# Performance work log

Hardware: AMD Instinct MI355X
Metric: run time of the kernel (lower is better)

## Reference

```python
import jax, jax.numpy as jnp
import numpy as np

# Graph geometry: G complete graphs (molecules) of n nodes each.
N_PER_G, G, DEG = 64, 256, 16
H, D = 8, 8
IN_DIM = H * D      # 64
EDGE_DIM = 64
N = N_PER_G * G                      # 16384 nodes
EF = G * N_PER_G * N_PER_G           # 1,048,576 full edges
ES = G * N_PER_G * DEG               # 262,144 sparse edges
SCALE = float(np.sqrt(D))


def _edges():
    n = N_PER_G
    # full graph: all (i -> j) pairs per block, edge id = b*n*n + i*n + j
    ij = np.arange(n * n)
    i, j = ij // n, ij % n
    b = np.arange(G)[:, None]
    src_full = (b * n + i[None, :]).reshape(-1).astype(np.int32)
    dst_full = (b * n + j[None, :]).reshape(-1).astype(np.int32)
    # sparse graph: each dst j receives from DEG distinct sources (j+1..j+DEG mod n)
    jj = np.arange(n)[:, None]
    kk = np.arange(DEG)[None, :]
    ii = (jj + 1 + kk) % n
    eid_block = (ii * n + jj).reshape(-1)                 # [n*DEG]
    sparse_eid = (np.arange(G)[:, None] * n * n + eid_block[None, :]).reshape(-1).astype(np.int32)
    return jnp.asarray(src_full), jnp.asarray(dst_full), jnp.asarray(sparse_eid)


def setup_inputs() -> dict:
    key = jax.random.key(0)
    ks = jax.random.split(key, 16)
    w = lambda k, shape, s=0.05: s * jax.random.normal(k, shape, jnp.float32)
    src_full, dst_full, sparse_eid = _edges()
    return dict(
        h=jax.random.normal(ks[0], (N, IN_DIM), jnp.float32),
        e=jax.random.normal(ks[1], (ES, EDGE_DIM), jnp.float32),
        adj2=jax.random.uniform(ks[2], (EF,), jnp.float32),
        rel_pos_3d=jax.random.normal(ks[3], (EF, H), jnp.float32),
        Wq=w(ks[4], (H * D, IN_DIM)), bq=jnp.zeros((H * D,), jnp.float32),
        Wk=w(ks[5], (H * D, IN_DIM)), bk=jnp.zeros((H * D,), jnp.float32),
        Wv=w(ks[6], (H * D, IN_DIM)), bv=jnp.zeros((H * D,), jnp.float32),
        Wpe=w(ks[7], (H, EDGE_DIM)), bpe=jnp.zeros((H,), jnp.float32),
        Wap=w(ks[8], (EDGE_DIM, H)), bap=jnp.zeros((EDGE_DIM,), jnp.float32),
        Wo=w(ks[9], (H * D, H * D)), bo=jnp.zeros((H * D,), jnp.float32),
        Woe=w(ks[10], (EDGE_DIM, EDGE_DIM)), boe=jnp.zeros((EDGE_DIM,), jnp.float32),
        src_full=src_full, dst_full=dst_full, sparse_eid=sparse_eid,
    )


def reference(h, e, adj2, rel_pos_3d, Wq, bq, Wk, bk, Wv, bv, Wpe, bpe,
              Wap, bap, Wo, bo, Woe, boe, src_full, dst_full, sparse_eid):
    Qh = (h @ Wq.T + bq).reshape(N, H, D)
    Kh = (h @ Wk.T + bk).reshape(N, H, D)
    Vh = (h @ Wv.T + bv).reshape(N, H, D)
    proj_e = e @ Wpe.T + bpe                                   # [ES, H]
    # edge-wise QK dot (src=K, dst=Q), scaled, then gaussian-decay + rel-pos bias
    score = jnp.sum(Kh[src_full] * Qh[dst_full], axis=-1) / SCALE   # [EF, H]
    score = score * adj2[:, None] + rel_pos_3d                      # [EF, H]
    # gather sparse-subgraph scores, project for edge output, add proj_e bias
    sc_sp = score[sparse_eid]                                        # [ES, H]
    e_out_raw = sc_sp @ Wap.T + bap                                  # [ES, EDGE_DIM]
    score = score.at[sparse_eid].set(sc_sp + proj_e)
    # edge softmax over incoming edges of each destination node
    logits = jnp.clip(score, -5.0, 5.0)
    m = jax.ops.segment_max(logits, dst_full, num_segments=N)
    ex = jnp.exp(logits - m[dst_full])
    den = jax.ops.segment_sum(ex, dst_full, num_segments=N)
    attn = ex / den[dst_full]                                        # [EF, H]
    # weighted scatter-sum of source values
    wV = jax.ops.segment_sum(Vh[src_full] * attn[..., None], dst_full, num_segments=N)
    h_out = wV.reshape(N, H * D) @ Wo.T + bo
    e_out = (e_out_raw + e) @ Woe.T + boe
    return h_out, e_out
```

## Files before the change

### kernel.cpp

```cpp
#include <hip/hip_runtime.h>


__global__ __launch_bounds__(512, 2) void qkvpe_kernel(
    const float* __restrict__ h,
    const float* __restrict__ e,
    const float* __restrict__ Wq, const float* __restrict__ bq,
    const float* __restrict__ Wk, const float* __restrict__ bk,
    const float* __restrict__ Wv, const float* __restrict__ bv,
    const float* __restrict__ Wpe, const float* __restrict__ bpe,
    float* __restrict__ Qs, float* __restrict__ Ks, float* __restrict__ Vs,
    float* __restrict__ PEs)
{
    const int t = threadIdx.x;
    if (blockIdx.x < 256) {
        const int b    = blockIdx.x;
        const int lane = t & 63;
        const int wu   = __builtin_amdgcn_readfirstlane(t >> 6);
        const float* hrow = h + (size_t)(b * 64 + lane) * 64;
        float accQ[8], accK[8], accV[8];
        #pragma unroll
        for (int cc = 0; cc < 8; ++cc) {
            const int c = wu * 8 + cc;
            accQ[cc] = bq[c]; accK[cc] = bk[c]; accV[cc] = bv[c];
        }
        #pragma unroll 1
        for (int k0 = 0; k0 < 4; ++k0) {
            float hv[16];
            #pragma unroll
            for (int u = 0; u < 4; ++u) {
                const float4 x = ((const float4*)hrow)[k0 * 4 + u];
                hv[u*4+0] = x.x; hv[u*4+1] = x.y; hv[u*4+2] = x.z; hv[u*4+3] = x.w;
            }
            #pragma unroll
            for (int cc = 0; cc < 8; ++cc) {
                const int c = wu * 8 + cc;
                const float* wq  = Wq + c * 64 + k0 * 16;
                const float* wk  = Wk + c * 64 + k0 * 16;
                const float* wvp = Wv + c * 64 + k0 * 16;
                #pragma unroll
                for (int k = 0; k < 16; ++k) {
                    accQ[cc] = fmaf(hv[k], wq[k],  accQ[cc]);
                    accK[cc] = fmaf(hv[k], wk[k],  accK[cc]);
                    accV[cc] = fmaf(hv[k], wvp[k], accV[cc]);
                }
            }
        }
        const size_t o = (size_t)(b * 64 + lane) * 64 + wu * 8;
        *(float4*)(Qs + o)     = make_float4(accQ[0], accQ[1], accQ[2], accQ[3]);
        *(float4*)(Qs + o + 4) = make_float4(accQ[4], accQ[5], accQ[6], accQ[7]);
        *(float4*)(Ks + o)     = make_float4(accK[0], accK[1], accK[2], accK[3]);
        *(float4*)(Ks + o + 4) = make_float4(accK[4], accK[5], accK[6], accK[7]);
        *(float4*)(Vs + o)     = make_float4(accV[0], accV[1], accV[2], accV[3]);
        *(float4*)(Vs + o + 4) = make_float4(accV[4], accV[5], accV[6], accV[7]);
    } else {
        const int row = (blockIdx.x - 256) * 512 + t;
        const float* erow = e + (size_t)row * 64;
        float acc[8];
        #pragma unroll
        for (int h2 = 0; h2 < 8; ++h2) acc[h2] = bpe[h2];
        #pragma unroll 1
        for (int k0 = 0; k0 < 4; ++k0) {
            float ev[16];
            #pragma unroll
            for (int u = 0; u < 4; ++u) {
                const float4 x = ((const float4*)erow)[k0 * 4 + u];
                ev[u*4+0] = x.x; ev[u*4+1] = x.y; ev[u*4+2] = x.z; ev[u*4+3] = x.w;
            }
            #pragma unroll
            for (int h2 = 0; h2 < 8; ++h2) {
                const float* wp = Wpe + h2 * 64 + k0 * 16;
                #pragma unroll
                for (int k = 0; k < 16; ++k)
                    acc[h2] = fmaf(ev[k], wp[k], acc[h2]);
            }
        }
        float* p0 = PEs + (size_t)row * 8;
        *(float4*)(p0)     = make_float4(acc[0], acc[1], acc[2], acc[3]);
        *(float4*)(p0 + 4) = make_float4(acc[4], acc[5], acc[6], acc[7]);
    }
}

__global__ __launch_bounds__(512, 2) void attn_kernel(
    const float* __restrict__ Qs, const float* __restrict__ Ks,
    const float* __restrict__ Vs, const float* __restrict__ PEs,
    const float* __restrict__ adj2,
    const float* __restrict__ rel,
    const float* __restrict__ Wo, const float* __restrict__ bo,
    float* __restrict__ h_out,
    float* __restrict__ scsp)
{
    __shared__ float shK[64 * 64];
    __shared__ float shV[64 * 64];
    __shared__ float shPE[512 * 8];

    const int b2   = blockIdx.x;
    const int b    = b2 >> 1;
    const int joff = (b2 & 1) << 5;
    const int t    = threadIdx.x;

    const int j_local = t >> 4;
    const int hh      = (t >> 1) & 7;
    const int half    = t & 1;
    const int j       = joff + j_local;

    const float* adjB = adj2 + (size_t)b * 4096 + j;
    const float* relB = rel  + ((size_t)b * 4096 + j) * 8 + hh;
    float A[32], R[32];
    #pragma unroll
    for (int it = 0; it < 32; ++it) {
        const int i = (half << 5) + it;
        A[it] = adjB[(size_t)i * 64];
        R[it] = relB[(size_t)i * 512];
    }

    {
        const int r = t >> 3, g = t & 7;
        const int d = r * 64 + ((g ^ (r & 7)) << 3);
        const float* kp = Ks + (size_t)b * 4096 + t * 8;
        const float* vp = Vs + (size_t)b * 4096 + t * 8;
        *(float4*)&shK[d]     = *(const float4*)(kp);
        *(float4*)&shK[d + 4] = *(const float4*)(kp + 4);
        *(float4*)&shV[d]     = *(const float4*)(vp);
        *(float4*)&shV[d + 4] = *(const float4*)(vp + 4);
        const float* pp = PEs + ((size_t)b * 1024 + joff * 16 + t) * 8;
        *(float4*)&shPE[t * 8]     = *(const float4*)(pp);
        *(float4*)&shPE[t * 8 + 4] = *(const float4*)(pp + 4);
    }
    float q[8];
    {
        const float* qp = Qs + (size_t)(b * 64 + j) * 64 + hh * 8;
        const float4 a = *(const float4*)qp;
        const float4 c = *(const float4*)(qp + 4);
        q[0]=a.x; q[1]=a.y; q[2]=a.z; q[3]=a.w;
        q[4]=c.x; q[5]=c.y; q[6]=c.z; q[7]=c.w;
    }
    __syncthreads();

    float den = 0.f;
    float wv[8] = {0.f,0.f,0.f,0.f,0.f,0.f,0.f,0.f};
    const float inv_scale = 0.35355339059327379f;
    #pragma unroll 4
    for (int it = 0; it < 32; ++it) {
        const int i  = (half << 5) + it;
        const int kb = i * 64 + ((hh ^ (i & 7)) << 3);
        const float4 kA = *(const float4*)&shK[kb];
        const float4 kB = *(const float4*)&shK[kb + 4];
        float s;
        s = kA.x * q[0];
        s = fmaf(kA.y, q[1], s); s = fmaf(kA.z, q[2], s); s = fmaf(kA.w, q[3], s);
        s = fmaf(kB.x, q[4], s); s = fmaf(kB.y, q[5], s); s = fmaf(kB.z, q[6], s);
        s = fmaf(kB.w, q[7], s);
        s = fmaf(s * inv_scale, A[it], R[it]);
        const int kidx = (i - j - 1) & 63;
        if (kidx < 16) {
            const int x = (j_local * 16 + kidx) * 8 + hh;
            const float pe = shPE[x];
            shPE[x] = s;
            s += pe;
        }
        s = fminf(fmaxf(s, -5.f), 5.f);
        const float ex = __expf(s);
        den += ex;
        const float4 vA = *(const float4*)&shV[kb];
        const float4 vB = *(const float4*)&shV[kb + 4];
        wv[0] = fmaf(ex, vA.x, wv[0]); wv[1] = fmaf(ex, vA.y, wv[1]);
        wv[2] = fmaf(ex, vA.z, wv[2]); wv[3] = fmaf(ex, vA.w, wv[3]);
        wv[4] = fmaf(ex, vB.x, wv[4]); wv[5] = fmaf(ex, vB.y, wv[5]);
        wv[6] = fmaf(ex, vB.z, wv[6]); wv[7] = fmaf(ex, vB.w, wv[7]);
    }
    den += __shfl_xor(den, 1);
    #pragma unroll
    for (int u = 0; u < 8; ++u) wv[u] += __shfl_xor(wv[u], 1);
    __syncthreads();

    {
        const float4 a = *(const float4*)&shPE[t * 8];
        const float4 c = *(const float4*)&shPE[t * 8 + 4];
        float* sp = scsp + (size_t)((size_t)b * 1024 + joff * 16 + t) * 8;
        *(float4*)(sp)     = a;
        *(float4*)(sp + 4) = c;
    }
    if (half == 0) {
        const float id = 1.f / den;
        float* wp = &shK[j_local * 64 + hh * 8];
        *(float4*)(wp)     = make_float4(wv[0]*id, wv[1]*id, wv[2]*id, wv[3]*id);
        *(float4*)(wp + 4) = make_float4(wv[4]*id, wv[5]*id, wv[6]*id, wv[7]*id);
    }
    __syncthreads();

    {
        const int rl = t >> 4;
        const int cq = t & 15;
        float acc[4];
        #pragma unroll
        for (int u = 0; u < 4; ++u) acc[u] = bo[cq * 4 + u];
        float tv[64];
        #pragma unroll
        for (int v = 0; v < 16; ++v) {
            const float4 x = *(const float4*)&shK[rl * 64 + v * 4];
            tv[v*4+0] = x.x; tv[v*4+1] = x.y; tv[v*4+2] = x.z; tv[v*4+3] = x.w;
        }
        #pragma unroll
        for (int u = 0; u < 4; ++u) {
            const float* wo = Wo + (cq * 4 + u) * 64;
            #pragma unroll
            for (int k = 0; k < 64; ++k)
                acc[u] = fmaf(tv[k], wo[k], acc[u]);
        }
        float* orow = h_out + (size_t)(b * 64 + joff + rl) * 64 + cq * 4;
        *(float4*)orow = make_float4(acc[0], acc[1], acc[2], acc[3]);
    }
}

__global__ void prep_kernel(const float* __restrict__ Wap, const float* __restrict__ bap,
                            const float* __restrict__ Woe, const float* __restrict__ boe,
                            float* __restrict__ M2)
{
    const int t = blockIdx.x * 64 + threadIdx.x;
    if (t < 512) {
        const int c = t >> 3, hq = t & 7;
        float s = 0.f;
        #pragma unroll 8
        for (int k = 0; k < 64; ++k) s = fmaf(Woe[c * 64 + k], Wap[k * 8 + hq], s);
        M2[t] = s;
    } else if (t < 576) {
        const int c = t - 512;
        float s = boe[c];
        #pragma unroll 8
        for (int k = 0; k < 64; ++k) s = fmaf(bap[k], Woe[t * 64 + k], s);
        M2[512 + c] = s;
    }
}

__global__ __launch_bounds__(256, 2) void eout_kernel(
    const float* __restrict__ e,
    const float* __restrict__ scsp,
    const float* __restrict__ Woe,
    const float* __restrict__ M2g,
    float* __restrict__ e_out)
{
    __shared__ float shE[64 * 64];
    __shared__ float shS[64 * 8];

    const int t    = threadIdx.x;
    const int base = blockIdx.x * 64;

    {
        const int r = t >> 2, qq = t & 3;
        const float* ep = e + (size_t)(base + r) * 64 + qq * 16;
        #pragma unroll
        for (int u = 0; u < 4; ++u) {
            const float4 x = ((const float4*)ep)[u];
            const int cc = qq * 4 + u;
            *(float4*)&shE[r * 64 + ((cc ^ (r & 15)) << 2)] = x;
        }
    }
    if (t < 128) {
        const int r = t >> 1, pp = t & 1;
        *(float4*)&shS[r * 8 + pp * 4] =
            *(const float4*)(scsp + (size_t)(base + r) * 8 + pp * 4);
    }
    __syncthreads();

    const int w = __builtin_amdgcn_readfirstlane(t >> 6);
    const int r = t & 63;

    float ev[64];
    #pragma unroll
    for (int v = 0; v < 16; ++v) {
        const float4 x = *(const float4*)&shE[r * 64 + ((v ^ (r & 15)) << 2)];
        ev[v*4+0] = x.x; ev[v*4+1] = x.y; ev[v*4+2] = x.z; ev[v*4+3] = x.w;
    }
    float sc[8];
    {
        const float4 a  = *(const float4*)&shS[r * 8];
        const float4 c4 = *(const float4*)&shS[r * 8 + 4];
        sc[0]=a.x; sc[1]=a.y; sc[2]=a.z; sc[3]=a.w;
        sc[4]=c4.x; sc[5]=c4.y; sc[6]=c4.z; sc[7]=c4.w;
    }
    float acc[16];
    #pragma unroll
    for (int u = 0; u < 16; ++u) {
        const int c = w * 16 + u;
        float s = M2g[512 + c];
        #pragma unroll
        for (int hq = 0; hq < 8; ++hq)
            s = fmaf(sc[hq], M2g[c * 8 + hq], s);
        acc[u] = s;
    }
    #pragma unroll
    for (int u = 0; u < 16; ++u) {
        const float* wr = Woe + (w * 16 + u) * 64;
        #pragma unroll
        for (int k = 0; k < 64; ++k)
            acc[u] = fmaf(ev[k], wr[k], acc[u]);
    }
    float* orow = e_out + (size_t)(base + r) * 64 + w * 16;
    #pragma unroll
    for (int u = 0; u < 4; ++u)
        *(float4*)&orow[u * 4] =
            make_float4(acc[u*4+0], acc[u*4+1], acc[u*4+2], acc[u*4+3]);
}

extern "C" void kernel_launch(void* const* d_in, const int* in_sizes, int n_in,
                              void* d_out, int out_size, void* d_ws, size_t ws_size,
                              hipStream_t stream) {
    const float* h    = (const float*)d_in[0];
    const float* e    = (const float*)d_in[1];
    const float* adj2 = (const float*)d_in[2];
    const float* rel  = (const float*)d_in[3];
    const float* Wq   = (const float*)d_in[4];  const float* bq  = (const float*)d_in[5];
    const float* Wk   = (const float*)d_in[6];  const float* bk  = (const float*)d_in[7];
    const float* Wv   = (const float*)d_in[8];  const float* bv  = (const float*)d_in[9];
    const float* Wpe  = (const float*)d_in[10]; const float* bpe = (const float*)d_in[11];
    const float* Wap  = (const float*)d_in[12]; const float* bap = (const float*)d_in[13];
    const float* Wo   = (const float*)d_in[14]; const float* bo  = (const float*)d_in[15];
    const float* Woe  = (const float*)d_in[16]; const float* boe = (const float*)d_in[17];

    float* out  = (float*)d_out;
    float* hout = out;
    float* eout = out + 16384 * 64;
    float* Qs   = eout;
    float* Ks   = eout + 1048576;
    float* Vs   = eout + 2097152;
    float* PEs  = eout + 3145728;
    float* ws   = (float*)d_ws;
    float* scsp = ws;
    float* M2g  = ws + 2097152;

    prep_kernel<<<dim3(9), dim3(64), 0, stream>>>(Wap, bap, Woe, boe, M2g);
    qkvpe_kernel<<<dim3(768), dim3(512), 0, stream>>>(
        h, e, Wq, bq, Wk, bk, Wv, bv, Wpe, bpe, Qs, Ks, Vs, PEs);
    attn_kernel<<<dim3(512), dim3(512), 0, stream>>>(
        Qs, Ks, Vs, PEs, adj2, rel, Wo, bo, hout, scsp);
    eout_kernel<<<dim3(4096), dim3(256), 0, stream>>>(e, scsp, Woe, M2g, eout);
}
```

Before: 148.2 us.

## Double attn_kernel threads to 1024, splitting source loop four ways per head

The attention kernel now runs 1024 threads per block. Each (dst, head) pair is split across four lanes of 16 sources each, with an extra shuffle level to combine partial sums. The A/R register preload is replaced by per-iteration global loads of adj2 and rel_pos, shared-memory staging is spread over more threads, and the Wo projection gives each thread two output columns in k-chunks to cut register pressure. The intent is more latency hiding and occupancy, at the cost of scalar staging loads and less ILP per thread. A prep_kernel indexing bug for the bias row of Woe is also fixed.

```diff
diff --git a/kernel.cpp b/kernel.cpp
--- a/kernel.cpp
+++ b/kernel.cpp
@@ -80,7 +80,7 @@
     }
 }
 
-__global__ __launch_bounds__(512, 2) void attn_kernel(
+__global__ __launch_bounds__(1024, 2) void attn_kernel(
     const float* __restrict__ Qs, const float* __restrict__ Ks,
     const float* __restrict__ Vs, const float* __restrict__ PEs,
     const float* __restrict__ adj2,
@@ -98,33 +98,27 @@
     const int joff = (b2 & 1) << 5;
     const int t    = threadIdx.x;
 
-    const int j_local = t >> 4;
-    const int hh      = (t >> 1) & 7;
-    const int half    = t & 1;
+    const int j_local = t >> 5;
+    const int hh      = (t >> 2) & 7;
+    const int q4      = t & 3;
     const int j       = joff + j_local;
 
-    const float* adjB = adj2 + (size_t)b * 4096 + j;
-    const float* relB = rel  + ((size_t)b * 4096 + j) * 8 + hh;
-    float A[32], R[32];
-    #pragma unroll
-    for (int it = 0; it < 32; ++it) {
-        const int i = (half << 5) + it;
-        A[it] = adjB[(size_t)i * 64];
-        R[it] = relB[(size_t)i * 512];
-    }
-
-    {
-        const int r = t >> 3, g = t & 7;
-        const int d = r * 64 + ((g ^ (r & 7)) << 3);
-        const float* kp = Ks + (size_t)b * 4096 + t * 8;
-        const float* vp = Vs + (size_t)b * 4096 + t * 8;
-        *(float4*)&shK[d]     = *(const float4*)(kp);
-        *(float4*)&shK[d + 4] = *(const float4*)(kp + 4);
-        *(float4*)&shV[d]     = *(const float4*)(vp);
-        *(float4*)&shV[d + 4] = *(const float4*)(vp + 4);
-        const float* pp = PEs + ((size_t)b * 1024 + joff * 16 + t) * 8;
-        *(float4*)&shPE[t * 8]     = *(const float4*)(pp);
-        *(float4*)&shPE[t * 8 + 4] = *(const float4*)(pp + 4);
+    {
+        const int r  = t >> 4;
+        const int gh = t & 15;
+        const int g  = gh >> 1, lo = (gh & 1) * 4;
+        const int d  = r * 64 + ((g ^ (r & 7)) << 3) + lo;
+        const int so = r * 64 + g * 8 + lo;
+        shK[d + 0] = Ks[(size_t)b * 4096 + so + 0];
+        shK[d + 1] = Ks[(size_t)b * 4096 + so + 1];
+        shK[d + 2] = Ks[(size_t)b * 4096 + so + 2];
+        shK[d + 3] = Ks[(size_t)b * 4096 + so + 3];
+        shV[d + 0] = Vs[(size_t)b * 4096 + so + 0];
+        shV[d + 1] = Vs[(size_t)b * 4096 + so + 1];
+        shV[d + 2] = Vs[(size_t)b * 4096 + so + 2];
+        shV[d + 3] = Vs[(size_t)b * 4096 + so + 3];
+        *(float4*)&shPE[t * 4] =
+            *(const float4*)(PEs + ((size_t)b * 1024 + joff * 16) * 8 + t * 4);
     }
     float q[8];
     {
@@ -138,10 +132,14 @@
 
     float den = 0.f;
     float wv[8] = {0.f,0.f,0.f,0.f,0.f,0.f,0.f,0.f};
+    const float* adjB = adj2 + (size_t)b * 4096 + j;
+    const float* relB = rel  + ((size_t)b * 4096 + j) * 8 + hh;
     const float inv_scale = 0.35355339059327379f;
     #pragma unroll 4
-    for (int it = 0; it < 32; ++it) {
-        const int i  = (half << 5) + it;
+    for (int it = 0; it < 16; ++it) {
+        const int i  = (q4 << 4) + it;
+        const float a2 = adjB[(size_t)i * 64];
+        const float rp = relB[(size_t)i * 512];
         const int kb = i * 64 + ((hh ^ (i & 7)) << 3);
         const float4 kA = *(const float4*)&shK[kb];
         const float4 kB = *(const float4*)&shK[kb + 4];
@@ -150,7 +148,7 @@
         s = fmaf(kA.y, q[1], s); s = fmaf(kA.z, q[2], s); s = fmaf(kA.w, q[3], s);
         s = fmaf(kB.x, q[4], s); s = fmaf(kB.y, q[5], s); s = fmaf(kB.z, q[6], s);
         s = fmaf(kB.w, q[7], s);
-        s = fmaf(s * inv_scale, A[it], R[it]);
+        s = fmaf(s * inv_scale, a2, rp);
         const int kidx = (i - j - 1) & 63;
         if (kidx < 16) {
             const int x = (j_local * 16 + kidx) * 8 + hh;
@@ -169,18 +167,20 @@
         wv[6] = fmaf(ex, vB.z, wv[6]); wv[7] = fmaf(ex, vB.w, wv[7]);
     }
     den += __shfl_xor(den, 1);
-    #pragma unroll
-    for (int u = 0; u < 8; ++u) wv[u] += __shfl_xor(wv[u], 1);
+    den += __shfl_xor(den, 2);
+    #pragma unroll
+    for (int u = 0; u < 8; ++u) {
+        wv[u] += __shfl_xor(wv[u], 1);
+        wv[u] += __shfl_xor(wv[u], 2);
+    }
     __syncthreads();
 
     {
-        const float4 a = *(const float4*)&shPE[t * 8];
-        const float4 c = *(const float4*)&shPE[t * 8 + 4];
-        float* sp = scsp + (size_t)((size_t)b * 1024 + joff * 16 + t) * 8;
-        *(float4*)(sp)     = a;
-        *(float4*)(sp + 4) = c;
-    }
-    if (half == 0) {
+        const int row = t >> 1, pp = t & 1;
+        *(float4*)(scsp + (size_t)((size_t)b * 1024 + joff * 16 + row) * 8 + pp * 4) =
+            *(const float4*)&shPE[row * 8 + pp * 4];
+    }
+    if (q4 == 0) {
         const float id = 1.f / den;
         float* wp = &shK[j_local * 64 + hh * 8];
         *(float4*)(wp)     = make_float4(wv[0]*id, wv[1]*id, wv[2]*id, wv[3]*id);
@@ -189,26 +189,28 @@
     __syncthreads();
 
     {
-        const int rl = t >> 4;
-        const int cq = t & 15;
-        float acc[4];
-        #pragma unroll
-        for (int u = 0; u < 4; ++u) acc[u] = bo[cq * 4 + u];
-        float tv[64];
-        #pragma unroll
-        for (int v = 0; v < 16; ++v) {
-            const float4 x = *(const float4*)&shK[rl * 64 + v * 4];
-            tv[v*4+0] = x.x; tv[v*4+1] = x.y; tv[v*4+2] = x.z; tv[v*4+3] = x.w;
-        }
-        #pragma unroll
-        for (int u = 0; u < 4; ++u) {
-            const float* wo = Wo + (cq * 4 + u) * 64;
-            #pragma unroll
-            for (int k = 0; k < 64; ++k)
-                acc[u] = fmaf(tv[k], wo[k], acc[u]);
-        }
-        float* orow = h_out + (size_t)(b * 64 + joff + rl) * 64 + cq * 4;
-        *(float4*)orow = make_float4(acc[0], acc[1], acc[2], acc[3]);
+        const int rl = t >> 5;
+        const int c0 = (t & 31) * 2;
+        float acc[2];
+        acc[0] = bo[c0]; acc[1] = bo[c0 + 1];
+        #pragma unroll 1
+        for (int k0 = 0; k0 < 4; ++k0) {
+            float tv[16];
+            #pragma unroll
+            for (int u = 0; u < 4; ++u) {
+                const float4 x = *(const float4*)&shK[rl * 64 + k0 * 16 + u * 4];
+                tv[u*4+0] = x.x; tv[u*4+1] = x.y; tv[u*4+2] = x.z; tv[u*4+3] = x.w;
+            }
+            #pragma unroll
+            for (int u = 0; u < 2; ++u) {
+                const float* wo = Wo + (c0 + u) * 64 + k0 * 16;
+                #pragma unroll
+                for (int k = 0; k < 16; ++k)
+                    acc[u] = fmaf(tv[k], wo[k], acc[u]);
+            }
+        }
+        float* orow = h_out + (size_t)(b * 64 + joff + rl) * 64 + c0;
+        *(float2*)orow = make_float2(acc[0], acc[1]);
     }
 }
 
@@ -227,7 +229,7 @@
         const int c = t - 512;
         float s = boe[c];
         #pragma unroll 8
-        for (int k = 0; k < 64; ++k) s = fmaf(bap[k], Woe[t * 64 + k], s);
+        for (int k = 0; k < 64; ++k) s = fmaf(bap[k], Woe[c * 64 + k], s);
         M2[512 + c] = s;
     }
 }
@@ -331,7 +333,7 @@
     prep_kernel<<<dim3(9), dim3(64), 0, stream>>>(Wap, bap, Woe, boe, M2g);
     qkvpe_kernel<<<dim3(768), dim3(512), 0, stream>>>(
         h, e, Wq, bq, Wk, bk, Wv, bv, Wpe, bpe, Qs, Ks, Vs, PEs);
-    attn_kernel<<<dim3(512), dim3(512), 0, stream>>>(
+    attn_kernel<<<dim3(512), dim3(1024), 0, stream>>>(
         Qs, Ks, Vs, PEs, adj2, rel, Wo, bo, hout, scsp);
     eout_kernel<<<dim3(4096), dim3(256), 0, stream>>>(e, scsp, Woe, M2g, eout);
 }
```

Result: no change. 145.3 us (-1.9%).
